# Performance work log

Measured on AMD Instinct MI355X. Metric: run time of the kernel, lower is better.

Reference implementation:

```python
import jax, jax.numpy as jnp
import numpy as np

B, S, D, H = 2, 2048, 2048, 16
HD = D // H  # 128


def setup_inputs() -> dict:
    key = jax.random.key(0)
    ks = jax.random.split(key, 9)
    s = 1.0 / np.sqrt(D)
    return {
        "x": jax.random.normal(ks[0], (B, S, D), dtype=jnp.float32),
        "Wq_w": jax.random.uniform(ks[1], (D, D), jnp.float32, -s, s),
        "Wq_b": jax.random.uniform(ks[2], (D,), jnp.float32, -s, s),
        "Wk_w": jax.random.uniform(ks[3], (HD, D), jnp.float32, -s, s),
        "Wk_b": jax.random.uniform(ks[4], (HD,), jnp.float32, -s, s),
        "Wv_w": jax.random.uniform(ks[5], (HD, D), jnp.float32, -s, s),
        "Wv_b": jax.random.uniform(ks[6], (HD,), jnp.float32, -s, s),
        "Wo_w": jax.random.uniform(ks[7], (D, D), jnp.float32, -s, s),
        "Wo_b": jax.random.uniform(ks[8], (D,), jnp.float32, -s, s),
    }


def reference(x, Wq_w, Wq_b, Wk_w, Wk_b, Wv_w, Wv_b, Wo_w, Wo_b):
    b, s, d = x.shape
    h, hd = H, HD
    # projections (torch Linear: x @ W.T + b)
    q = (x @ Wq_w.T + Wq_b).reshape(b, s, h, hd).transpose(0, 2, 1, 3)  # (b,h,s,hd)
    k = x @ Wk_w.T + Wk_b  # (b,s,hd) single shared KV head
    v = x @ Wv_w.T + Wv_b  # (b,s,hd)
    scores = jnp.einsum("bhsd,btd->bhst", q, k) / jnp.sqrt(jnp.float32(hd))
    attn = jax.nn.softmax(scores, axis=-1)
    out = jnp.einsum("bhst,btd->bhsd", attn, v)  # (b,h,s,hd)
    # faithful to original: reshape WITHOUT transposing heads back
    out = out.reshape(b, s, d)
    return out @ Wo_w.T + Wo_b
```

## Files before the change

kernel.cpp:

```cpp
#include <hip/hip_runtime.h>
#include <stdint.h>

#define BATCH 2
#define SEQ   2048
#define DMOD  2048
#define NHEAD 16
#define HDIM  128

typedef __bf16 bf16x8 __attribute__((ext_vector_type(8)));
typedef float f32x4   __attribute__((ext_vector_type(4)));
typedef float f32x16  __attribute__((ext_vector_type(16)));
typedef unsigned short u16x8 __attribute__((ext_vector_type(8)));

#define MFMA16(a, b, c) __builtin_amdgcn_mfma_f32_16x16x32_bf16(a, b, c, 0, 0, 0)
#define MFMA32(a, b, c) __builtin_amdgcn_mfma_f32_32x32x16_bf16(a, b, c, 0, 0, 0)

__device__ __forceinline__ uint16_t f2bf(float f) {
  union { float f; uint32_t u; } cv; cv.f = f;
  uint32_t u = cv.u;
  return (uint16_t)((u + 0x7FFFu + ((u >> 16) & 1u)) >> 16);
}

__device__ __forceinline__ float fexp2(float x) { return exp2f(x); }

__device__ __forceinline__ uint32_t pkbf(float a, float b) {
  uint32_t d;
  asm("v_cvt_pk_bf16_f32 %0, %1, %2" : "=v"(d) : "v"(a), "v"(b));
  return d;
}

__device__ __forceinline__ void gload_lds16(const void* g, void* l) {
  __builtin_amdgcn_global_load_lds(
      (__attribute__((address_space(1))) void*)g,
      (__attribute__((address_space(3))) void*)l, 16, 0, 0);
}

__global__ __launch_bounds__(256) void cvtbf16(const float* __restrict__ in,
                                               uint16_t* __restrict__ out, int n) {
  int i = (blockIdx.x * 256 + threadIdx.x) * 8;
  if (i >= n) return;
  f32x4 a = *(const f32x4*)&in[i];
  f32x4 b = *(const f32x4*)&in[i + 4];
  u16x8 o;
  o[0] = f2bf(a[0]); o[1] = f2bf(a[1]); o[2] = f2bf(a[2]); o[3] = f2bf(a[3]);
  o[4] = f2bf(b[0]); o[5] = f2bf(b[1]); o[6] = f2bf(b[2]); o[7] = f2bf(b[3]);
  *(u16x8*)&out[i] = o;
}

template <bool OUT_F32, bool HAS_KV>
__global__ __launch_bounds__(512, 1) void gemm8(
    const uint16_t* __restrict__ A,
    const uint16_t* __restrict__ Bw, const float* __restrict__ bias,
    void* __restrict__ out, int ldc, float oscale,
    const uint16_t* __restrict__ Bkv,
    const float* __restrict__ biask, const float* __restrict__ biasv,
    uint16_t* __restrict__ kout, uint16_t* __restrict__ vout) {
  extern __shared__ uint16_t smem[];
  uint16_t* As = smem;
  uint16_t* Bs = smem + 3 * 128 * 64;

  const int lane = threadIdx.x & 63, w = threadIdx.x >> 6;
  const int half = lane >> 4, fr = lane & 15;
  const int wr = w >> 2, wc = w & 3;

  const int f = blockIdx.x;
  bool kvblk = false;
  int m0, n0;
  const uint16_t* Bb;
  if (HAS_KV && f >= 256) {
    kvblk = true; m0 = (f - 256) * 128; n0 = 0; Bb = Bkv;
  } else {
    const int xcd = f & 7, idx = f >> 3;
    const int mblk = (xcd >> 1) * 8 + (idx & 7);
    const int nblk = (xcd & 1) * 4 + (idx >> 3);
    m0 = mblk * 128; n0 = nblk * 256; Bb = Bw;
  }

  const int rsub = lane >> 3;
  const int swcol = ((lane & 7) ^ rsub) * 8;
  const size_t a0 = (size_t)(m0 + (2 * w) * 8 + rsub) * DMOD + swcol;
  const size_t b0 = (size_t)(n0 + (4 * w) * 8 + rsub) * DMOD + swcol;

  f32x4 acc[4][4] = {};
  const int NT = DMOD / 64;

  auto STAGE = [&](int kt, int slot) {
    uint16_t* Ad = As + slot * (128 * 64);
    uint16_t* Bd = Bs + slot * (256 * 64);
    const int kk = kt * 64;
    gload_lds16(&A[a0 + kk],            &Ad[(2 * w) * 512]);
    gload_lds16(&A[a0 + 8 * DMOD + kk], &Ad[(2 * w + 1) * 512]);
    gload_lds16(&Bb[b0 + kk],             &Bd[(4 * w) * 512]);
    gload_lds16(&Bb[b0 + 8 * DMOD + kk],  &Bd[(4 * w + 1) * 512]);
    gload_lds16(&Bb[b0 + 16 * DMOD + kk], &Bd[(4 * w + 2) * 512]);
    gload_lds16(&Bb[b0 + 24 * DMOD + kk], &Bd[(4 * w + 3) * 512]);
  };

  STAGE(0, 0);
  STAGE(1, 1);
  asm volatile("s_waitcnt vmcnt(6)" ::: "memory");
  __builtin_amdgcn_s_barrier();
  asm volatile("" ::: "memory");

  int sc_ = 0, ss_ = 2;
#pragma unroll 1
  for (int t = 0; t < NT; ++t) {
    if (t + 2 < NT) STAGE(t + 2, ss_);

    const uint16_t* Ar = As + sc_ * (128 * 64);
    const uint16_t* Br = Bs + sc_ * (256 * 64);
#pragma unroll
    for (int kc = 0; kc < 2; ++kc) {
      bf16x8 af[4], bf[4];
      const int slot = ((kc * 4 + half) ^ (fr & 7)) * 8;
#pragma unroll
      for (int i = 0; i < 4; ++i)
        af[i] = *(const bf16x8*)&Ar[(wr * 64 + i * 16 + fr) * 64 + slot];
#pragma unroll
      for (int j = 0; j < 4; ++j)
        bf[j] = *(const bf16x8*)&Br[(wc * 64 + j * 16 + fr) * 64 + slot];
      __builtin_amdgcn_s_setprio(1);
#pragma unroll
      for (int i = 0; i < 4; ++i)
#pragma unroll
        for (int j = 0; j < 4; ++j)
          acc[i][j] = MFMA16(af[i], bf[j], acc[i][j]);
      __builtin_amdgcn_s_setprio(0);
    }

    if (t + 2 < NT) asm volatile("s_waitcnt vmcnt(6)" ::: "memory");
    else            asm volatile("s_waitcnt vmcnt(0)" ::: "memory");
    if (t + 1 < NT) {
      __builtin_amdgcn_s_barrier();
      asm volatile("" ::: "memory");
    }
    sc_ = (sc_ == 2) ? 0 : sc_ + 1;
    ss_ = (ss_ == 2) ? 0 : ss_ + 1;
  }

  const float os = kvblk ? 1.0f : oscale;
#pragma unroll
  for (int j = 0; j < 4; ++j) {
    const int col = wc * 64 + j * 16 + fr;
    float bv_;
    if (!kvblk) bv_ = bias[n0 + col];
    else        bv_ = (col < 128) ? biask[col] : biasv[col - 128];
#pragma unroll
    for (int i = 0; i < 4; ++i) {
      const int rowb = m0 + wr * 64 + i * 16 + half * 4;
#pragma unroll
      for (int r = 0; r < 4; ++r) {
        const float v = (acc[i][j][r] + bv_) * os;
        if (!kvblk) {
          if (OUT_F32) ((float*)out)[(size_t)(rowb + r) * ldc + n0 + col] = v;
          else ((uint16_t*)out)[(size_t)(rowb + r) * ldc + n0 + col] = f2bf(v);
        } else {
          if (col < 128) kout[(size_t)(rowb + r) * HDIM + col] = f2bf(v);
          else           vout[(size_t)(rowb + r) * HDIM + col - 128] = f2bf(v);
        }
      }
    }
  }
}

__global__ __launch_bounds__(256) void transpose_v(const uint16_t* __restrict__ vb,
                                                   uint16_t* __restrict__ vt) {
  __shared__ uint16_t tile[64][65];
  const int s0 = blockIdx.x * 64, d0 = blockIdx.y * 64, b = blockIdx.z;
  const int tx = threadIdx.x & 63, ty = threadIdx.x >> 6;
#pragma unroll
  for (int r = ty; r < 64; r += 4)
    tile[r][tx] = vb[((size_t)b * SEQ + s0 + r) * HDIM + d0 + tx];
  __syncthreads();
#pragma unroll
  for (int r = ty; r < 64; r += 4)
    vt[((size_t)b * HDIM + d0 + r) * SEQ + s0 + tx] = tile[tx][r];
}

__global__ __launch_bounds__(256, 2) void mqa_attn(
    const uint16_t* __restrict__ qb,
    const uint16_t* __restrict__ kb,
    const uint16_t* __restrict__ vt,
    uint16_t* __restrict__ ab) {
  __shared__ uint16_t Ks[2][64 * 128];
  __shared__ uint16_t Vs[2][128 * 64];

  const int t = threadIdx.x, lane = t & 63, w = t >> 6;
  const int l31 = lane & 31, hi = lane >> 5;
  const int qt = blockIdx.x, h = blockIdx.y, b = blockIdx.z;
  const size_t rowbase = (size_t)b * SEQ;
  const int q0 = qt * 128 + w * 32;

  bf16x8 qf[8];
  {
    const uint16_t* qrow = &qb[(rowbase + q0 + l31) * DMOD + h * HDIM + hi * 8];
#pragma unroll
    for (int c8 = 0; c8 < 8; ++c8)
      qf[c8] = *(const bf16x8*)&qrow[c8 * 16];
  }

  f32x16 ot[4] = {};
  float lsum = 0.f;

  const int skrow = lane >> 4;
  const int skcol = (lane & 15) * 8;
  const int svrow = lane >> 3;
  const int svcol = (lane & 7) * 8;

#pragma unroll
  for (int c = 0; c < 4; ++c) {
    const int ch = c * 4 + w;
    const int krow = ch * 4 + skrow;
    gload_lds16(&kb[(rowbase + krow) * HDIM + (skcol ^ ((krow & 7) << 3))],
                &Ks[0][ch * 512]);
    const int vrow = ch * 8 + svrow;
    gload_lds16(&vt[((size_t)b * HDIM + vrow) * SEQ + (svcol ^ ((vrow & 7) << 3))],
                &Vs[0][ch * 512]);
  }
  __syncthreads();

  for (int kt = 0; kt < SEQ / 64; ++kt) {
    const int cur = kt & 1;
    if (kt < SEQ / 64 - 1) {
#pragma unroll
      for (int c = 0; c < 4; ++c) {
        const int ch = c * 4 + w;
        const int krow = ch * 4 + skrow;
        gload_lds16(&kb[(rowbase + (kt + 1) * 64 + krow) * HDIM +
                        (skcol ^ ((krow & 7) << 3))],
                    &Ks[cur ^ 1][ch * 512]);
        const int vrow = ch * 8 + svrow;
        gload_lds16(&vt[((size_t)b * HDIM + vrow) * SEQ + (kt + 1) * 64 +
                        (svcol ^ ((vrow & 7) << 3))],
                    &Vs[cur ^ 1][ch * 512]);
      }
    }

    f32x16 st[2] = {};
    __builtin_amdgcn_s_setprio(1);
#pragma unroll
    for (int c8 = 0; c8 < 8; ++c8) {
#pragma unroll
      for (int tt = 0; tt < 2; ++tt) {
        const int krow = tt * 32 + l31;
        bf16x8 kf = *(const bf16x8*)&Ks[cur][krow * 128 +
                        ((c8 * 16 + hi * 8) ^ ((krow & 7) << 3))];
        st[tt] = MFMA32(kf, qf[c8], st[tt]);
      }
    }
    __builtin_amdgcn_s_setprio(0);

    uint32_t wk[2][8];
    float s = 0.f;
#pragma unroll
    for (int tt = 0; tt < 2; ++tt) {
      float e[16];
#pragma unroll
      for (int i = 0; i < 16; ++i) {
        e[i] = fexp2(st[tt][i]);
        s += e[i];
      }
#pragma unroll
      for (int i = 0; i < 8; ++i)
        wk[tt][i] = pkbf(e[2 * i], e[2 * i + 1]);
    }
    s += __shfl_xor(s, 32);
    lsum += s;

    bf16x8 pf[4];
#pragma unroll
    for (int tt = 0; tt < 2; ++tt) {
      uint32_t a0 = wk[tt][0], c0 = wk[tt][2];
      uint32_t a1 = wk[tt][1], c1 = wk[tt][3];
      uint32_t a2 = wk[tt][4], c2 = wk[tt][6];
      uint32_t a3 = wk[tt][5], c3 = wk[tt][7];
      asm volatile("v_permlane32_swap_b32 %0, %1" : "+v"(a0), "+v"(c0));
      asm volatile("v_permlane32_swap_b32 %0, %1" : "+v"(a1), "+v"(c1));
      asm volatile("v_permlane32_swap_b32 %0, %1" : "+v"(a2), "+v"(c2));
      asm volatile("v_permlane32_swap_b32 %0, %1" : "+v"(a3), "+v"(c3));
      union { uint32_t u[4]; bf16x8 v; } p0, p1;
      p0.u[0] = a0; p0.u[1] = a1; p0.u[2] = c0; p0.u[3] = c1;
      p1.u[0] = a2; p1.u[1] = a3; p1.u[2] = c2; p1.u[3] = c3;
      pf[2 * tt] = p0.v;
      pf[2 * tt + 1] = p1.v;
    }

    __builtin_amdgcn_s_setprio(1);
#pragma unroll
    for (int kc = 0; kc < 4; ++kc) {
#pragma unroll
      for (int dt = 0; dt < 4; ++dt) {
        const int vrow = dt * 32 + l31;
        bf16x8 vf = *(const bf16x8*)&Vs[cur][vrow * 64 +
                        ((kc * 16 + hi * 8) ^ ((vrow & 7) << 3))];
        ot[dt] = MFMA32(vf, pf[kc], ot[dt]);
      }
    }
    __builtin_amdgcn_s_setprio(0);

    __syncthreads();
  }

  const float inv = 1.f / lsum;
  const size_t orow = ((size_t)(b * NHEAD + h) * SEQ + q0 + l31) * HDIM;
#pragma unroll
  for (int dt = 0; dt < 4; ++dt)
#pragma unroll
    for (int qd = 0; qd < 4; ++qd) {
      ushort4 hv;
      hv.x = f2bf(ot[dt][qd * 4 + 0] * inv);
      hv.y = f2bf(ot[dt][qd * 4 + 1] * inv);
      hv.z = f2bf(ot[dt][qd * 4 + 2] * inv);
      hv.w = f2bf(ot[dt][qd * 4 + 3] * inv);
      *(ushort4*)&ab[orow + dt * 32 + qd * 8 + hi * 4] = hv;
    }
}

extern "C" void kernel_launch(void* const* d_in, const int* in_sizes, int n_in,
                              void* d_out, int out_size, void* d_ws, size_t ws_size,
                              hipStream_t stream) {
  const float* x    = (const float*)d_in[0];
  const float* Wq_w = (const float*)d_in[1];
  const float* Wq_b = (const float*)d_in[2];
  const float* Wk_w = (const float*)d_in[3];
  const float* Wk_b = (const float*)d_in[4];
  const float* Wv_w = (const float*)d_in[5];
  const float* Wv_b = (const float*)d_in[6];
  const float* Wo_w = (const float*)d_in[7];
  const float* Wo_b = (const float*)d_in[8];
  float* out = (float*)d_out;

  char* ws = (char*)d_ws;
  uint16_t* xb  = (uint16_t*)(ws + 0);
  uint16_t* ab  = xb;
  uint16_t* wqb = (uint16_t*)(ws + 16777216);
  uint16_t* vt  = wqb;
  uint16_t* wkb = (uint16_t*)(ws + 25165824);
  uint16_t* wvb = (uint16_t*)(ws + 25690112);
  uint16_t* wob = (uint16_t*)(ws + 26214400);
  uint16_t* qb  = (uint16_t*)(ws + 34603008);
  uint16_t* kb  = (uint16_t*)(ws + 51380224);
  uint16_t* vb  = (uint16_t*)(ws + 52428800);

  const float qscale = 0.08838834764831845f * 1.4426950408889634f;
  const int GEMM_LDS = 3 * (128 + 256) * 64 * 2;

  hipFuncSetAttribute(reinterpret_cast<const void*>(gemm8<false, true>),
                      hipFuncAttributeMaxDynamicSharedMemorySize, GEMM_LDS);
  hipFuncSetAttribute(reinterpret_cast<const void*>(gemm8<true, false>),
                      hipFuncAttributeMaxDynamicSharedMemorySize, GEMM_LDS);

  cvtbf16<<<4096, 256, 0, stream>>>(x, xb, BATCH * SEQ * DMOD);
  cvtbf16<<<2048, 256, 0, stream>>>(Wq_w, wqb, DMOD * DMOD);
  cvtbf16<<<128, 256, 0, stream>>>(Wk_w, wkb, HDIM * DMOD);
  cvtbf16<<<128, 256, 0, stream>>>(Wv_w, wvb, HDIM * DMOD);
  cvtbf16<<<2048, 256, 0, stream>>>(Wo_w, wob, DMOD * DMOD);

  gemm8<false, true><<<288, 512, GEMM_LDS, stream>>>(
      xb, wqb, Wq_b, qb, DMOD, qscale, wkb, Wk_b, Wv_b, kb, vb);
  transpose_v<<<dim3(32, 2, 2), 256, 0, stream>>>(vb, vt);
  mqa_attn<<<dim3(16, 16, 2), 256, 0, stream>>>(qb, kb, vt, ab);
  gemm8<true, false><<<256, 512, GEMM_LDS, stream>>>(
      ab, wob, Wo_b, out, DMOD, 1.0f, nullptr, nullptr, nullptr, nullptr, nullptr);
}
```

Before: 317.2 us.

## Fuse QKV into one retiled GEMM and share K/V tiles across heads

Measured after the change: 292.7 us. 7.7% less time.

```diff
diff --git a/kernel.cpp b/kernel.cpp
--- a/kernel.cpp
+++ b/kernel.cpp
@@ -6,6 +6,7 @@
 #define DMOD  2048
 #define NHEAD 16
 #define HDIM  128
+#define QKVN  2304
 
 typedef __bf16 bf16x8 __attribute__((ext_vector_type(8)));
 typedef float f32x4   __attribute__((ext_vector_type(4)));
@@ -47,14 +48,101 @@
   *(u16x8*)&out[i] = o;
 }
 
-template <bool OUT_F32, bool HAS_KV>
-__global__ __launch_bounds__(512, 1) void gemm8(
+__global__ __launch_bounds__(512, 4) void qkv_gemm2(
+    const uint16_t* __restrict__ A,
+    const uint16_t* __restrict__ W,
+    const float* __restrict__ bq, const float* __restrict__ bk,
+    const float* __restrict__ bv,
+    uint16_t* __restrict__ out,
+    float qscale) {
+  extern __shared__ uint16_t smem[];
+  uint16_t* As = smem;
+  uint16_t* Bs = smem + 2 * 128 * 64;
+
+  const int lane = threadIdx.x & 63, w = threadIdx.x >> 6;
+  const int half = lane >> 4, fr = lane & 15;
+  const int wr = w >> 2, wc = w & 3;
+
+  const int f = blockIdx.x;
+  const int m0 = (f & 31) * 128;
+  const int n0 = (f >> 5) * 192;
+
+  const int rsub = lane >> 3;
+  const int swcol = ((lane & 7) ^ rsub) * 8;
+  const size_t a0 = (size_t)(m0 + 2 * w * 8 + rsub) * DMOD + swcol;
+  const size_t b0 = (size_t)(n0 + 3 * w * 8 + rsub) * DMOD + swcol;
+
+  f32x4 acc[4][3] = {};
+  const int NT = DMOD / 64;
+
+  auto STAGE = [&](int kt, int buf) {
+    uint16_t* Ad = As + buf * (128 * 64);
+    uint16_t* Bd = Bs + buf * (192 * 64);
+    const int kk = kt * 64;
+    gload_lds16(&A[a0 + kk],            &Ad[(2 * w) * 512]);
+    gload_lds16(&A[a0 + 8 * DMOD + kk], &Ad[(2 * w + 1) * 512]);
+    gload_lds16(&W[b0 + kk],             &Bd[(3 * w) * 512]);
+    gload_lds16(&W[b0 + 8 * DMOD + kk],  &Bd[(3 * w + 1) * 512]);
+    gload_lds16(&W[b0 + 16 * DMOD + kk], &Bd[(3 * w + 2) * 512]);
+  };
+
+  STAGE(0, 0);
+  asm volatile("s_waitcnt vmcnt(0)" ::: "memory");
+  __builtin_amdgcn_s_barrier();
+
+#pragma unroll 1
+  for (int t = 0; t < NT; ++t) {
+    const int cur = t & 1;
+    if (t + 1 < NT) STAGE(t + 1, cur ^ 1);
+
+    const uint16_t* Ar = As + cur * (128 * 64);
+    const uint16_t* Br = Bs + cur * (192 * 64);
+#pragma unroll
+    for (int kc = 0; kc < 2; ++kc) {
+      bf16x8 af[4], bf[3];
+      const int slot = ((kc * 4 + half) ^ (fr & 7)) * 8;
+#pragma unroll
+      for (int i = 0; i < 4; ++i)
+        af[i] = *(const bf16x8*)&Ar[(wr * 64 + i * 16 + fr) * 64 + slot];
+#pragma unroll
+      for (int j = 0; j < 3; ++j)
+        bf[j] = *(const bf16x8*)&Br[(wc * 48 + j * 16 + fr) * 64 + slot];
+      __builtin_amdgcn_s_setprio(1);
+#pragma unroll
+      for (int i = 0; i < 4; ++i)
+#pragma unroll
+        for (int j = 0; j < 3; ++j)
+          acc[i][j] = MFMA16(af[i], bf[j], acc[i][j]);
+      __builtin_amdgcn_s_setprio(0);
+    }
+
+    if (t + 1 < NT) {
+      asm volatile("s_waitcnt vmcnt(0)" ::: "memory");
+      __builtin_amdgcn_s_barrier();
+    }
+  }
+
+#pragma unroll
+  for (int j = 0; j < 3; ++j) {
+    const int col = n0 + wc * 48 + j * 16 + fr;
+    float bv_, os_;
+    if (col < DMOD)            { bv_ = bq[col];        os_ = qscale; }
+    else if (col < DMOD + 128) { bv_ = bk[col - DMOD]; os_ = 1.0f; }
+    else                       { bv_ = bv[col - DMOD - 128]; os_ = 1.0f; }
+#pragma unroll
+    for (int i = 0; i < 4; ++i) {
+      const int rowb = m0 + wr * 64 + i * 16 + half * 4;
+#pragma unroll
+      for (int r = 0; r < 4; ++r)
+        out[(size_t)(rowb + r) * QKVN + col] = f2bf((acc[i][j][r] + bv_) * os_);
+    }
+  }
+}
+
+__global__ __launch_bounds__(512, 1) void o_gemm(
     const uint16_t* __restrict__ A,
     const uint16_t* __restrict__ Bw, const float* __restrict__ bias,
-    void* __restrict__ out, int ldc, float oscale,
-    const uint16_t* __restrict__ Bkv,
-    const float* __restrict__ biask, const float* __restrict__ biasv,
-    uint16_t* __restrict__ kout, uint16_t* __restrict__ vout) {
+    float* __restrict__ out) {
   extern __shared__ uint16_t smem[];
   uint16_t* As = smem;
   uint16_t* Bs = smem + 3 * 128 * 64;
@@ -64,17 +152,8 @@
   const int wr = w >> 2, wc = w & 3;
 
   const int f = blockIdx.x;
-  bool kvblk = false;
-  int m0, n0;
-  const uint16_t* Bb;
-  if (HAS_KV && f >= 256) {
-    kvblk = true; m0 = (f - 256) * 128; n0 = 0; Bb = Bkv;
-  } else {
-    const int xcd = f & 7, idx = f >> 3;
-    const int mblk = (xcd >> 1) * 8 + (idx & 7);
-    const int nblk = (xcd & 1) * 4 + (idx >> 3);
-    m0 = mblk * 128; n0 = nblk * 256; Bb = Bw;
-  }
+  const int m0 = (f & 31) * 128;
+  const int n0 = (f >> 5) * 256;
 
   const int rsub = lane >> 3;
   const int swcol = ((lane & 7) ^ rsub) * 8;
@@ -90,17 +169,16 @@
     const int kk = kt * 64;
     gload_lds16(&A[a0 + kk],            &Ad[(2 * w) * 512]);
     gload_lds16(&A[a0 + 8 * DMOD + kk], &Ad[(2 * w + 1) * 512]);
-    gload_lds16(&Bb[b0 + kk],             &Bd[(4 * w) * 512]);
-    gload_lds16(&Bb[b0 + 8 * DMOD + kk],  &Bd[(4 * w + 1) * 512]);
-    gload_lds16(&Bb[b0 + 16 * DMOD + kk], &Bd[(4 * w + 2) * 512]);
-    gload_lds16(&Bb[b0 + 24 * DMOD + kk], &Bd[(4 * w + 3) * 512]);
+    gload_lds16(&Bw[b0 + kk],             &Bd[(4 * w) * 512]);
+    gload_lds16(&Bw[b0 + 8 * DMOD + kk],  &Bd[(4 * w + 1) * 512]);
+    gload_lds16(&Bw[b0 + 16 * DMOD + kk], &Bd[(4 * w + 2) * 512]);
+    gload_lds16(&Bw[b0 + 24 * DMOD + kk], &Bd[(4 * w + 3) * 512]);
   };
 
   STAGE(0, 0);
   STAGE(1, 1);
   asm volatile("s_waitcnt vmcnt(6)" ::: "memory");
   __builtin_amdgcn_s_barrier();
-  asm volatile("" ::: "memory");
 
   int sc_ = 0, ss_ = 2;
 #pragma unroll 1
@@ -130,56 +208,41 @@
 
     if (t + 2 < NT) asm volatile("s_waitcnt vmcnt(6)" ::: "memory");
     else            asm volatile("s_waitcnt vmcnt(0)" ::: "memory");
-    if (t + 1 < NT) {
-      __builtin_amdgcn_s_barrier();
-      asm volatile("" ::: "memory");
-    }
+    if (t + 1 < NT) __builtin_amdgcn_s_barrier();
     sc_ = (sc_ == 2) ? 0 : sc_ + 1;
     ss_ = (ss_ == 2) ? 0 : ss_ + 1;
   }
 
-  const float os = kvblk ? 1.0f : oscale;
 #pragma unroll
   for (int j = 0; j < 4; ++j) {
     const int col = wc * 64 + j * 16 + fr;
-    float bv_;
-    if (!kvblk) bv_ = bias[n0 + col];
-    else        bv_ = (col < 128) ? biask[col] : biasv[col - 128];
+    const float bv_ = bias[n0 + col];
 #pragma unroll
     for (int i = 0; i < 4; ++i) {
       const int rowb = m0 + wr * 64 + i * 16 + half * 4;
 #pragma unroll
-      for (int r = 0; r < 4; ++r) {
-        const float v = (acc[i][j][r] + bv_) * os;
-        if (!kvblk) {
-          if (OUT_F32) ((float*)out)[(size_t)(rowb + r) * ldc + n0 + col] = v;
-          else ((uint16_t*)out)[(size_t)(rowb + r) * ldc + n0 + col] = f2bf(v);
-        } else {
-          if (col < 128) kout[(size_t)(rowb + r) * HDIM + col] = f2bf(v);
-          else           vout[(size_t)(rowb + r) * HDIM + col - 128] = f2bf(v);
-        }
-      }
-    }
-  }
-}
-
-__global__ __launch_bounds__(256) void transpose_v(const uint16_t* __restrict__ vb,
+      for (int r = 0; r < 4; ++r)
+        out[(size_t)(rowb + r) * DMOD + n0 + col] = acc[i][j][r] + bv_;
+    }
+  }
+}
+
+__global__ __launch_bounds__(256) void transpose_v(const uint16_t* __restrict__ qkv,
                                                    uint16_t* __restrict__ vt) {
   __shared__ uint16_t tile[64][65];
   const int s0 = blockIdx.x * 64, d0 = blockIdx.y * 64, b = blockIdx.z;
   const int tx = threadIdx.x & 63, ty = threadIdx.x >> 6;
 #pragma unroll
   for (int r = ty; r < 64; r += 4)
-    tile[r][tx] = vb[((size_t)b * SEQ + s0 + r) * HDIM + d0 + tx];
+    tile[r][tx] = qkv[((size_t)b * SEQ + s0 + r) * QKVN + (DMOD + 128) + d0 + tx];
   __syncthreads();
 #pragma unroll
   for (int r = ty; r < 64; r += 4)
     vt[((size_t)b * HDIM + d0 + r) * SEQ + s0 + tx] = tile[tx][r];
 }
 
-__global__ __launch_bounds__(256, 2) void mqa_attn(
-    const uint16_t* __restrict__ qb,
-    const uint16_t* __restrict__ kb,
+__global__ __launch_bounds__(512, 2) void mqa_attn(
+    const uint16_t* __restrict__ qkv,
     const uint16_t* __restrict__ vt,
     uint16_t* __restrict__ ab) {
   __shared__ uint16_t Ks[2][64 * 128];
@@ -187,13 +250,14 @@
 
   const int t = threadIdx.x, lane = t & 63, w = t >> 6;
   const int l31 = lane & 31, hi = lane >> 5;
-  const int qt = blockIdx.x, h = blockIdx.y, b = blockIdx.z;
+  const int qt = blockIdx.x, hg = blockIdx.y, b = blockIdx.z;
+  const int h = hg * 8 + w;
   const size_t rowbase = (size_t)b * SEQ;
-  const int q0 = qt * 128 + w * 32;
+  const int q0 = qt * 32;
 
   bf16x8 qf[8];
   {
-    const uint16_t* qrow = &qb[(rowbase + q0 + l31) * DMOD + h * HDIM + hi * 8];
+    const uint16_t* qrow = &qkv[(rowbase + q0 + l31) * QKVN + h * HDIM + hi * 8];
 #pragma unroll
     for (int c8 = 0; c8 < 8; ++c8)
       qf[c8] = *(const bf16x8*)&qrow[c8 * 16];
@@ -208,10 +272,10 @@
   const int svcol = (lane & 7) * 8;
 
 #pragma unroll
-  for (int c = 0; c < 4; ++c) {
-    const int ch = c * 4 + w;
+  for (int c = 0; c < 2; ++c) {
+    const int ch = 2 * w + c;
     const int krow = ch * 4 + skrow;
-    gload_lds16(&kb[(rowbase + krow) * HDIM + (skcol ^ ((krow & 7) << 3))],
+    gload_lds16(&qkv[(rowbase + krow) * QKVN + DMOD + (skcol ^ ((krow & 7) << 3))],
                 &Ks[0][ch * 512]);
     const int vrow = ch * 8 + svrow;
     gload_lds16(&vt[((size_t)b * HDIM + vrow) * SEQ + (svcol ^ ((vrow & 7) << 3))],
@@ -223,11 +287,11 @@
     const int cur = kt & 1;
     if (kt < SEQ / 64 - 1) {
 #pragma unroll
-      for (int c = 0; c < 4; ++c) {
-        const int ch = c * 4 + w;
+      for (int c = 0; c < 2; ++c) {
+        const int ch = 2 * w + c;
         const int krow = ch * 4 + skrow;
-        gload_lds16(&kb[(rowbase + (kt + 1) * 64 + krow) * HDIM +
-                        (skcol ^ ((krow & 7) << 3))],
+        gload_lds16(&qkv[(rowbase + (kt + 1) * 64 + krow) * QKVN + DMOD +
+                         (skcol ^ ((krow & 7) << 3))],
                     &Ks[cur ^ 1][ch * 512]);
         const int vrow = ch * 8 + svrow;
         gload_lds16(&vt[((size_t)b * HDIM + vrow) * SEQ + (kt + 1) * 64 +
@@ -331,24 +395,23 @@
   float* out = (float*)d_out;
 
   char* ws = (char*)d_ws;
-  uint16_t* xb  = (uint16_t*)(ws + 0);
-  uint16_t* ab  = xb;
-  uint16_t* wqb = (uint16_t*)(ws + 16777216);
-  uint16_t* vt  = wqb;
-  uint16_t* wkb = (uint16_t*)(ws + 25165824);
-  uint16_t* wvb = (uint16_t*)(ws + 25690112);
-  uint16_t* wob = (uint16_t*)(ws + 26214400);
-  uint16_t* qb  = (uint16_t*)(ws + 34603008);
-  uint16_t* kb  = (uint16_t*)(ws + 51380224);
-  uint16_t* vb  = (uint16_t*)(ws + 52428800);
+  uint16_t* xb    = (uint16_t*)(ws + 0);
+  uint16_t* ab    = xb;
+  uint16_t* wqb   = (uint16_t*)(ws + 16777216);
+  uint16_t* vt    = wqb;
+  uint16_t* wkb   = (uint16_t*)(ws + 25165824);
+  uint16_t* wvb   = (uint16_t*)(ws + 25690112);
+  uint16_t* wob   = (uint16_t*)(ws + 26214400);
+  uint16_t* qkv_u = (uint16_t*)(ws + 34603008);
 
   const float qscale = 0.08838834764831845f * 1.4426950408889634f;
-  const int GEMM_LDS = 3 * (128 + 256) * 64 * 2;
-
-  hipFuncSetAttribute(reinterpret_cast<const void*>(gemm8<false, true>),
-                      hipFuncAttributeMaxDynamicSharedMemorySize, GEMM_LDS);
-  hipFuncSetAttribute(reinterpret_cast<const void*>(gemm8<true, false>),
-                      hipFuncAttributeMaxDynamicSharedMemorySize, GEMM_LDS);
+  const int QKV_LDS = 2 * (128 + 192) * 64 * 2;
+  const int O_LDS   = 3 * (128 + 256) * 64 * 2;
+
+  hipFuncSetAttribute(reinterpret_cast<const void*>(qkv_gemm2),
+                      hipFuncAttributeMaxDynamicSharedMemorySize, QKV_LDS);
+  hipFuncSetAttribute(reinterpret_cast<const void*>(o_gemm),
+                      hipFuncAttributeMaxDynamicSharedMemorySize, O_LDS);
 
   cvtbf16<<<4096, 256, 0, stream>>>(x, xb, BATCH * SEQ * DMOD);
   cvtbf16<<<2048, 256, 0, stream>>>(Wq_w, wqb, DMOD * DMOD);
@@ -356,10 +419,8 @@
   cvtbf16<<<128, 256, 0, stream>>>(Wv_w, wvb, HDIM * DMOD);
   cvtbf16<<<2048, 256, 0, stream>>>(Wo_w, wob, DMOD * DMOD);
 
-  gemm8<false, true><<<288, 512, GEMM_LDS, stream>>>(
-      xb, wqb, Wq_b, qb, DMOD, qscale, wkb, Wk_b, Wv_b, kb, vb);
-  transpose_v<<<dim3(32, 2, 2), 256, 0, stream>>>(vb, vt);
-  mqa_attn<<<dim3(16, 16, 2), 256, 0, stream>>>(qb, kb, vt, ab);
-  gemm8<true, false><<<256, 512, GEMM_LDS, stream>>>(
-      ab, wob, Wo_b, out, DMOD, 1.0f, nullptr, nullptr, nullptr, nullptr, nullptr);
-}
+  qkv_gemm2<<<384, 512, QKV_LDS, stream>>>(xb, wqb, Wq_b, Wk_b, Wv_b, qkv_u, qscale);
+  transpose_v<<<dim3(32, 2, 2), 256, 0, stream>>>(qkv_u, vt);
+  mqa_attn<<<dim3(64, 2, 2), 512, 0, stream>>>(qkv_u, vt, ab);
+  o_gemm<<<256, 512, O_LDS, stream>>>(ab, wob, Wo_b, out);
+}
```
